# Performance work log

Measured on AMD Instinct MI355X. Metric: run time of the kernel, lower is better.

The kernel has to match this reference:

```python
import jax, jax.numpy as jnp
import numpy as np

B, N, C, H = 8, 4096, 768, 32
D = C // H  # head_dim = 24
EPS = 1e-12


def _l2norm(t):
    # F.normalize(dim=-1): t / max(||t||_2, eps)
    n = jnp.sqrt(jnp.sum(t * t, axis=-1, keepdims=True))
    return t / jnp.maximum(n, EPS)


def setup_inputs() -> dict:
    key = jax.random.key(0)
    ks = jax.random.split(key, 6)
    s_in = 1.0 / np.sqrt(C)
    return {
        "x": jax.random.normal(ks[0], (B, N, C), dtype=jnp.float32),
        "W_qkv": jax.random.uniform(ks[1], (C, 3 * C), jnp.float32, -s_in, s_in),
        "b_qkv": jax.random.uniform(ks[2], (3 * C,), jnp.float32, -s_in, s_in),
        "temperature": jnp.ones((H, 1, 1), dtype=jnp.float32),
        "W_proj": jax.random.uniform(ks[3], (C, C), jnp.float32, -s_in, s_in),
        "b_proj": jax.random.uniform(ks[4], (C,), jnp.float32, -s_in, s_in),
    }


def reference(x, W_qkv, b_qkv, temperature, W_proj, b_proj):
    b, n, c = x.shape
    qkv = x @ W_qkv + b_qkv                                  # (B,N,3C)
    qkv = qkv.reshape(b, n, 3, H, D).transpose(2, 0, 3, 1, 4)  # (3,B,H,N,D)
    q, k, v = qkv[0], qkv[1], qkv[2]                         # (B,H,N,D)
    q = jnp.swapaxes(q, -1, -2)                              # (B,H,D,N)
    k = jnp.swapaxes(k, -1, -2)
    v = jnp.swapaxes(v, -1, -2)
    q = _l2norm(q)                                           # normalize over N
    k = _l2norm(k)
    attn = jnp.einsum('bhdn,bhen->bhde', q, k) * temperature  # (B,H,D,D)
    attn = jax.nn.softmax(attn, axis=-1)
    y = jnp.einsum('bhde,bhen->bhdn', attn, v)               # (B,H,D,N)
    # Faithful to torch: (1,B,H,D,N).transpose(1,2).reshape(B,N,C)
    # == (H,B,D,N) flattened row-major into (B,N,C)
    y = jnp.transpose(y, (1, 0, 2, 3)).reshape(b, n, c)
    return y @ W_proj + b_proj
```

## Files before the change

kernel.cpp:

```cpp
#include <hip/hip_runtime.h>
#include <hip/hip_bf16.h>


#define DEVI __device__ __forceinline__

typedef __attribute__((ext_vector_type(8))) short bf16x8;
typedef __attribute__((ext_vector_type(4))) float f32x4;
typedef unsigned int u32;
typedef unsigned short u16;

DEVI u16 f2bf(float f) {
  union { float f; u32 u; } x; x.f = f;
  u32 r = x.u + 0x7FFFu + ((x.u >> 16) & 1u);
  return (u16)(r >> 16);
}

DEVI void gload_lds16(const void* g, void* l) {
  __builtin_amdgcn_global_load_lds((__attribute__((address_space(1))) void*)g,
                                   (__attribute__((address_space(3))) void*)l, 16, 0, 0);
}

__global__ __launch_bounds__(256) void cvt_kernel(const float* __restrict__ in,
                                                  u16* __restrict__ out, int n8) {
  int i = blockIdx.x * 256 + threadIdx.x;
  if (i >= n8) return;
  long o = (long)i * 8;
  float4 a = *(const float4*)(in + o);
  float4 b = *(const float4*)(in + o + 4);
  uint4 v;
  v.x = f2bf(a.x) | ((u32)f2bf(a.y) << 16);
  v.y = f2bf(a.z) | ((u32)f2bf(a.w) << 16);
  v.z = f2bf(b.x) | ((u32)f2bf(b.y) << 16);
  v.w = f2bf(b.z) | ((u32)f2bf(b.w) << 16);
  *(uint4*)(out + o) = v;
}

__global__ __launch_bounds__(256) void transpose_cvt(const float* __restrict__ W,
                                                     u16* __restrict__ Wt, int K, int N) {
  __shared__ float tile[32][33];
  int n0 = blockIdx.x * 32, k0 = blockIdx.y * 32;
  int tx = threadIdx.x, ty = threadIdx.y;
  #pragma unroll
  for (int i = 0; i < 4; ++i)
    tile[ty + 8 * i][tx] = W[(long)(k0 + ty + 8 * i) * N + n0 + tx];
  __syncthreads();
  #pragma unroll
  for (int i = 0; i < 4; ++i)
    Wt[(long)(n0 + ty + 8 * i) * K + k0 + tx] = f2bf(tile[tx][ty + 8 * i]);
}

template<int NT>
__global__ __launch_bounds__(256, 2) void gemm_w1_kernel(
    const u16* __restrict__ A, const u16* __restrict__ Bt,
    const float* __restrict__ bias, u16* __restrict__ Cout, int N) {
  constexpr int K = NT * 32;
  __shared__ __attribute__((aligned(128))) char lds[73728];

  int nbx = N >> 8;
  int nwg = gridDim.x;
  int bid = blockIdx.x;
  bid = (bid & 7) * (nwg >> 3) + (bid >> 3);
  int bx = bid % nbx, by = bid / nbx;

  int t = threadIdx.x;
  int w = t >> 6, l = t & 63;
  int wr = w >> 1, wc = w & 1;
  int l16 = l & 15, l4 = l >> 4;

  int cbb = (l4 * 16) ^ ((l16 & 8) << 2);
  int pA0 = (wr * 64 + l16) * 64 + cbb;
  int pB0 = (wc * 128 + l16) * 64 + cbb;

  int soffA[2], soffB[4];
  #pragma unroll
  for (int j = 0; j < 2; ++j) {
    int p = (j * 256 + t) * 16;
    int la = p ^ (((p >> 9) & 1) << 5);
    soffA[j] = (la >> 6) * K + ((la & 63) >> 1);
  }
  #pragma unroll
  for (int j = 0; j < 4; ++j) {
    int p = (j * 256 + t) * 16;
    int lb = p ^ (((p >> 9) & 1) << 5);
    soffB[j] = (lb >> 6) * K + ((lb & 63) >> 1);
  }

  const u16* Ag = A + (long)by * 128 * K;
  const u16* Bg = Bt + (long)bx * 256 * K;
  int sdst = w * 1024;

  f32x4 acc[4][8] = {};

#define STAGE_W1(ktile, slot)                                                  \
  { _Pragma("unroll") for (int j_ = 0; j_ < 2; ++j_)                           \
      gload_lds16(Ag + soffA[j_] + (ktile) * 32,                               \
                  lds + (slot) * 8192 + j_ * 4096 + sdst);                     \
    _Pragma("unroll") for (int j_ = 0; j_ < 4; ++j_)                           \
      gload_lds16(Bg + soffB[j_] + (ktile) * 32,                               \
                  lds + 24576 + (slot) * 16384 + j_ * 4096 + sdst); }

  STAGE_W1(0, 0);
  STAGE_W1(1, 1);

  #pragma unroll
  for (int kt = 0; kt < NT; ++kt) {
    int rs = kt % 3;
    if (kt + 2 < NT) {
      STAGE_W1(kt + 2, (kt + 2) % 3);
      asm volatile("s_waitcnt vmcnt(12)" ::: "memory");
    } else if (kt + 2 == NT) {
      asm volatile("s_waitcnt vmcnt(6)" ::: "memory");
    } else {
      asm volatile("s_waitcnt vmcnt(0)" ::: "memory");
    }
    __builtin_amdgcn_sched_barrier(0);
    __builtin_amdgcn_s_barrier();
    __builtin_amdgcn_sched_barrier(0);

    bf16x8 aF[4], bF[8];
    #pragma unroll
    for (int mi = 0; mi < 4; ++mi)
      aF[mi] = *(const bf16x8*)(lds + rs * 8192 + mi * 1024 + pA0);
    #pragma unroll
    for (int n = 0; n < 8; ++n)
      bF[n] = *(const bf16x8*)(lds + 24576 + rs * 16384 + n * 1024 + pB0);

    __builtin_amdgcn_s_setprio(1);
    #pragma unroll
    for (int mi = 0; mi < 4; ++mi)
      #pragma unroll
      for (int n = 0; n < 8; ++n)
        acc[mi][n] = __builtin_amdgcn_mfma_f32_16x16x32_bf16(aF[mi], bF[n], acc[mi][n], 0, 0, 0);
    __builtin_amdgcn_s_setprio(0);
    __builtin_amdgcn_s_barrier();
    __builtin_amdgcn_sched_barrier(0);
  }

  #pragma unroll
  for (int mi = 0; mi < 4; ++mi) {
    int row0 = by * 128 + wr * 64 + mi * 16 + l4 * 4;
    #pragma unroll
    for (int n = 0; n < 8; ++n) {
      int col = bx * 256 + wc * 128 + n * 16 + l16;
      float bv = bias[col];
      #pragma unroll
      for (int j = 0; j < 4; ++j) {
        long idx = (long)(row0 + j) * N + col;
        Cout[idx] = f2bf(acc[mi][n][j] + bv);
      }
    }
  }
#undef STAGE_W1
}

#define STAGE3(ktile, slot)                                                    \
  { _Pragma("unroll") for (int j_ = 0; j_ < 2; ++j_) {                         \
      gload_lds16(Ag + soffA[j_] + (ktile) * 32,                               \
                  lds + (slot) * 8192 + j_ * 4096 + sdst);                     \
      gload_lds16(Bg + soffB[j_] + (ktile) * 32,                               \
                  lds + 24576 + (slot) * 8192 + j_ * 4096 + sdst); } }

template<int NT>
__global__ __launch_bounds__(256, 3) void gemm3c_kernel(
    const u16* __restrict__ A, const u16* __restrict__ Bt,
    const float* __restrict__ bias, float* __restrict__ Cout,
    int M, int N) {
  constexpr int K = NT * 32;
  __shared__ __attribute__((aligned(128))) char lds[49152];

  int nbx = N >> 7;
  int nwg = gridDim.x;
  int bid = blockIdx.x;
  bid = (bid & 7) * (nwg >> 3) + (bid >> 3);
  int bx = bid % nbx, by = bid / nbx;

  int t = threadIdx.x;
  int w = t >> 6, l = t & 63;
  int wr = w >> 1, wc = w & 1;
  int l16 = l & 15, l4 = l >> 4;

  int cbb = (l4 * 16) ^ ((l16 & 8) << 2);
  int pA0 = (wr * 64 + l16) * 64 + cbb;
  int pB0 = (wc * 64 + l16) * 64 + cbb;

  int soffA[2], soffB[2];
  #pragma unroll
  for (int j = 0; j < 2; ++j) {
    int p = (j * 256 + t) * 16;
    int lb = p ^ (((p >> 9) & 1) << 5);
    soffA[j] = (lb >> 6) * K + ((lb & 63) >> 1);
    soffB[j] = soffA[j];
  }

  const u16* Ag = A + (long)by * 128 * K;
  const u16* Bg = Bt + (long)bx * 128 * K;
  int sdst = w * 1024;

  f32x4 acc[4][4] = {};

  STAGE3(0, 0);
  STAGE3(1, 1);

  #pragma unroll
  for (int kt = 0; kt < NT; ++kt) {
    int rs = kt % 3;
    if (kt + 2 < NT) {
      STAGE3(kt + 2, (kt + 2) % 3);
      asm volatile("s_waitcnt vmcnt(8)" ::: "memory");
    } else if (kt + 2 == NT) {
      asm volatile("s_waitcnt vmcnt(4)" ::: "memory");
    } else {
      asm volatile("s_waitcnt vmcnt(0)" ::: "memory");
    }
    __builtin_amdgcn_sched_barrier(0);
    __builtin_amdgcn_s_barrier();
    __builtin_amdgcn_sched_barrier(0);

    bf16x8 aF[4], bF[4];
    #pragma unroll
    for (int mi = 0; mi < 4; ++mi)
      aF[mi] = *(const bf16x8*)(lds + rs * 8192 + mi * 1024 + pA0);
    #pragma unroll
    for (int n = 0; n < 4; ++n)
      bF[n] = *(const bf16x8*)(lds + 24576 + rs * 8192 + n * 1024 + pB0);

    __builtin_amdgcn_s_setprio(1);
    #pragma unroll
    for (int mi = 0; mi < 4; ++mi)
      #pragma unroll
      for (int n = 0; n < 4; ++n)
        acc[mi][n] = __builtin_amdgcn_mfma_f32_16x16x32_bf16(aF[mi], bF[n], acc[mi][n], 0, 0, 0);
    __builtin_amdgcn_s_setprio(0);
    __builtin_amdgcn_s_barrier();
    __builtin_amdgcn_sched_barrier(0);
  }

  #pragma unroll
  for (int mi = 0; mi < 4; ++mi) {
    int row0 = by * 128 + wr * 64 + mi * 16 + l4 * 4;
    #pragma unroll
    for (int n = 0; n < 4; ++n) {
      int col = bx * 128 + wc * 64 + n * 16 + l16;
      float bv = bias[col];
      #pragma unroll
      for (int j = 0; j < 4; ++j) {
        long idx = (long)(row0 + j) * N + col;
        __builtin_nontemporal_store(acc[mi][n][j] + bv, Cout + idx);
      }
    }
  }
}

#define PFQK(nc, rq, rk)                                                       \
  { long cb = (long)(nc) * 589824;                                             \
    _Pragma("unroll") for (int i = 0; i < 3; ++i) {                            \
      rq[i] = *(const uint4*)(qbase + cb + offI[i]);                           \
      rk[i] = *(const uint4*)(kbase + cb + offI[i]); } }

#define WRQK(rq, rk)                                                           \
  { _Pragma("unroll") for (int i = 0; i < 3; ++i) {                            \
      const u32* pq = (const u32*)&rq[i];                                      \
      const u32* pk = (const u32*)&rk[i];                                      \
      _Pragma("unroll") for (int j = 0; j < 4; ++j) {                          \
        int d = sI[i] * 8 + 2 * j;                                             \
        qt[d][nI[i]] = (u16)pq[j]; qt[d + 1][nI[i]] = (u16)(pq[j] >> 16);      \
        kt[d][nI[i]] = (u16)pk[j]; kt[d + 1][nI[i]] = (u16)(pk[j] >> 16); } } }

#define GRAM8                                                                  \
  { _Pragma("unroll") for (int ks = 0; ks < 8; ++ks) {                         \
      int koff = ks * 32 + l4 * 8;                                             \
      bf16x8 qa = *(const bf16x8*)&qt[fm * 16 + l16][koff];                    \
      bf16x8 qb = *(const bf16x8*)&qt[fn * 16 + l16][koff];                    \
      bf16x8 ka = *(const bf16x8*)&kt[fm * 16 + l16][koff];                    \
      bf16x8 kb = *(const bf16x8*)&kt[fn * 16 + l16][koff];                    \
      accG = __builtin_amdgcn_mfma_f32_16x16x32_bf16(qa, kb, accG, 0, 0, 0);   \
      accQ = __builtin_amdgcn_mfma_f32_16x16x32_bf16(qa, qb, accQ, 0, 0, 0);   \
      accK = __builtin_amdgcn_mfma_f32_16x16x32_bf16(ka, kb, accK, 0, 0, 0); } }

__global__ __launch_bounds__(256) void gram_kernel(const u16* __restrict__ qkv,
                                                   float* __restrict__ gram) {
  __shared__ u16 qt[32][280];
  __shared__ u16 kt[32][280];

  int bid = blockIdx.x;
  int bh = bid >> 2, s = bid & 3;
  int b = bh >> 5, h = bh & 31;
  int t = threadIdx.x;
  int w = t >> 6, l = t & 63;
  int l16 = l & 15, l4 = l >> 4;
  int fm = w >> 1, fn = w & 1;

  for (int i = t; i < 32 * 280; i += 256) { qt[0][i] = 0; kt[0][i] = 0; }

  int nI[3], sI[3], offI[3];
  #pragma unroll
  for (int i = 0; i < 3; ++i) {
    int idx = t + 256 * i;
    nI[i] = idx / 3; sI[i] = idx % 3;
    offI[i] = nI[i] * 2304 + sI[i] * 8;
  }

  f32x4 accG = {}, accQ = {}, accK = {};
  const u16* qbase = qkv + (long)b * 4096 * 2304 + h * 24;
  const u16* kbase = qbase + 768;
  int c0 = s * 4;

  uint4 rq[3], rk[3];
  PFQK(c0, rq, rk);
  __syncthreads();

  #pragma unroll
  for (int c = 0; c < 4; ++c) {
    WRQK(rq, rk);
    __syncthreads();
    if (c + 1 < 4) PFQK(c0 + c + 1, rq, rk);
    GRAM8;
    __syncthreads();
  }

  float* gb = gram + (long)(bh * 4 + s) * 3072;
  int row = fm * 16 + l4 * 4, col = fn * 16 + l16;
  #pragma unroll
  for (int j = 0; j < 4; ++j) {
    gb[(row + j) * 32 + col] = accG[j];
    gb[1024 + (row + j) * 32 + col] = accQ[j];
    gb[2048 + (row + j) * 32 + col] = accK[j];
  }
}

__global__ __launch_bounds__(32) void softmax_kernel(const float* __restrict__ gram,
                                                     const float* __restrict__ temperature,
                                                     u16* __restrict__ attnb) {
  int bh = blockIdx.x;
  int h = bh & 31;
  int d = threadIdx.x;
  u16* ab = attnb + bh * 1024;
  if (d < 24) {
    const float* gb = gram + (long)bh * 12288;
    float nq2 = 0.f, row[24], nk2[24];
    #pragma unroll
    for (int e = 0; e < 24; ++e) { row[e] = 0.f; nk2[e] = 0.f; }
    #pragma unroll
    for (int s = 0; s < 4; ++s) {
      const float* gs = gb + s * 3072;
      nq2 += gs[1024 + d * 33];
      #pragma unroll
      for (int e = 0; e < 24; ++e) {
        row[e] += gs[d * 32 + e];
        nk2[e] += gs[2048 + e * 33];
      }
    }
    float nq = fmaxf(sqrtf(fmaxf(nq2, 0.f)), 1e-12f);
    float tmp = temperature[h];
    float mx = -1e30f;
    #pragma unroll
    for (int e = 0; e < 24; ++e) {
      float nk = fmaxf(sqrtf(fmaxf(nk2[e], 0.f)), 1e-12f);
      row[e] = row[e] / (nq * nk) * tmp;
      mx = fmaxf(mx, row[e]);
    }
    float ssum = 0.f;
    #pragma unroll
    for (int e = 0; e < 24; ++e) { row[e] = __expf(row[e] - mx); ssum += row[e]; }
    float inv = 1.f / ssum;
    #pragma unroll
    for (int e = 0; e < 24; ++e) ab[d * 32 + e] = f2bf(row[e] * inv);
    #pragma unroll
    for (int e = 24; e < 32; ++e) ab[d * 32 + e] = 0;
  } else {
    #pragma unroll
    for (int e = 0; e < 32; ++e) ab[d * 32 + e] = 0;
  }
}

__global__ __launch_bounds__(256) void pv_kernel(const u16* __restrict__ qkv,
                                                 const u16* __restrict__ attnb,
                                                 u16* __restrict__ yout) {
  __shared__ u16 vl[256][40];
  int bid = blockIdx.x;
  int bh = bid >> 4, c = bid & 15;
  int b = bh >> 5, h = bh & 31;
  int t = threadIdx.x;
  int w = t >> 6, l = t & 63;
  int l16 = l & 15, l4 = l >> 4;

  for (int i = t; i < 5120; i += 256) ((u32*)vl)[i] = 0;

  const u16* ab = attnb + bh * 1024;
  bf16x8 af0 = *(const bf16x8*)(ab + l16 * 32 + l4 * 8);
  bf16x8 af1 = *(const bf16x8*)(ab + (16 + l16) * 32 + l4 * 8);

  const u16* vbase = qkv + (long)b * 4096 * 2304 + h * 24 + 1536;
  uint4 rv[3];
  int nI[3], sI[3];
  #pragma unroll
  for (int i = 0; i < 3; ++i) {
    int idx = t + 256 * i;
    nI[i] = idx / 3; sI[i] = idx % 3;
    rv[i] = *(const uint4*)(vbase + (long)c * 589824 + nI[i] * 2304 + sI[i] * 8);
  }
  __syncthreads();
  #pragma unroll
  for (int i = 0; i < 3; ++i) *(uint4*)&vl[nI[i]][sI[i] * 8] = rv[i];
  __syncthreads();

  u16* ybase = yout + (long)(h * 8 + b) * 24 * 4096;
  int n0 = c * 256;
  f32x4 z = {};
  #pragma unroll
  for (int fnn = 0; fnn < 4; ++fnn) {
    int ncol = w * 64 + fnn * 16 + l16;
    bf16x8 bv = *(const bf16x8*)&vl[ncol][l4 * 8];
    f32x4 y0 = __builtin_amdgcn_mfma_f32_16x16x32_bf16(af0, bv, z, 0, 0, 0);
    f32x4 y1 = __builtin_amdgcn_mfma_f32_16x16x32_bf16(af1, bv, z, 0, 0, 0);
    int gn = n0 + ncol;
    #pragma unroll
    for (int j = 0; j < 4; ++j) {
      int d0 = l4 * 4 + j;
      ybase[(long)d0 * 4096 + gn] = f2bf(y0[j]);
      int d1 = 16 + d0;
      if (d1 < 24) ybase[(long)d1 * 4096 + gn] = f2bf(y1[j]);
    }
  }
}

extern "C" void kernel_launch(void* const* d_in, const int* in_sizes, int n_in,
                              void* d_out, int out_size, void* d_ws, size_t ws_size,
                              hipStream_t stream) {
  const float* x     = (const float*)d_in[0];
  const float* Wqkv  = (const float*)d_in[1];
  const float* bqkv  = (const float*)d_in[2];
  const float* temp  = (const float*)d_in[3];
  const float* Wproj = (const float*)d_in[4];
  const float* bproj = (const float*)d_in[5];
  float* out = (float*)d_out;

  char* ws = (char*)d_ws;
  u16*   xb    = (u16*)(ws);
  float* gram  = (float*)(ws);
  u16*   y     = (u16*)(ws);
  u16*   wqt   = (u16*)(ws + 50331648);
  u16*   attnb = (u16*)(ws + 50331648);
  u16*   wpt   = (u16*)(ws + 53870592);
  u16*   qkv   = (u16*)(ws + 55050240);

  cvt_kernel<<<12288, 256, 0, stream>>>(x, xb, 3145728);
  transpose_cvt<<<dim3(72, 24), dim3(32, 8), 0, stream>>>(Wqkv, wqt, 768, 2304);
  transpose_cvt<<<dim3(24, 24), dim3(32, 8), 0, stream>>>(Wproj, wpt, 768, 768);
  gemm_w1_kernel<24><<<2304, 256, 0, stream>>>(xb, wqt, bqkv, qkv, 2304);
  gram_kernel<<<1024, 256, 0, stream>>>(qkv, gram);
  softmax_kernel<<<256, 32, 0, stream>>>(gram, temp, attnb);
  pv_kernel<<<4096, 256, 0, stream>>>(qkv, attnb, y);
  gemm3c_kernel<24><<<1536, 256, 0, stream>>>(y, wpt, bproj, out, 32768, 768);
}
```

Baseline: 295.7 us.

## Use 512-thread QKV GEMM blocks and merge weight transpose launches

The QKV GEMM now runs 8 waves per block instead of 4 on the same 128x256 tile, so each wave computes 64x64 rather than 64x128. Accumulator registers are halved and the global-to-LDS staging work is spread across more threads. The two weight transpose-convert kernels are merged into one launch that picks Wqkv or Wproj from the block index. This trades fewer MFMAs per LDS fragment load, and so lower operand reuse, for more waves to hide latency, and it also saves one launch.

```diff
diff --git a/kernel.cpp b/kernel.cpp
--- a/kernel.cpp
+++ b/kernel.cpp
@@ -35,10 +35,16 @@
   *(uint4*)(out + o) = v;
 }
 
-__global__ __launch_bounds__(256) void transpose_cvt(const float* __restrict__ W,
-                                                     u16* __restrict__ Wt, int K, int N) {
+__global__ __launch_bounds__(256) void transpose_cvt2(const float* __restrict__ Wq,
+                                                      u16* __restrict__ Wqt,
+                                                      const float* __restrict__ Wp,
+                                                      u16* __restrict__ Wpt) {
   __shared__ float tile[32][33];
-  int n0 = blockIdx.x * 32, k0 = blockIdx.y * 32;
+  int bx = blockIdx.x;
+  const float* W; u16* Wt; int N, n0;
+  if (bx < 72) { W = Wq; Wt = Wqt; N = 2304; n0 = bx * 32; }
+  else         { W = Wp; Wt = Wpt; N = 768;  n0 = (bx - 72) * 32; }
+  int k0 = blockIdx.y * 32;
   int tx = threadIdx.x, ty = threadIdx.y;
   #pragma unroll
   for (int i = 0; i < 4; ++i)
@@ -46,13 +52,20 @@
   __syncthreads();
   #pragma unroll
   for (int i = 0; i < 4; ++i)
-    Wt[(long)(n0 + ty + 8 * i) * K + k0 + tx] = f2bf(tile[tx][ty + 8 * i]);
-}
+    Wt[(long)(n0 + ty + 8 * i) * 768 + k0 + tx] = f2bf(tile[tx][ty + 8 * i]);
+}
+
+#define STAGE_T(ktile, slot)                                                   \
+  { gload_lds16(Ag + soffA + (ktile) * 32, lds + (slot) * 8192 + sdst);        \
+    _Pragma("unroll") for (int j_ = 0; j_ < 2; ++j_)                           \
+      gload_lds16(Bg + soffB[j_] + (ktile) * 32,                               \
+                  lds + 24576 + (slot) * 16384 + j_ * 8192 + sdst); }
 
 template<int NT>
-__global__ __launch_bounds__(256, 2) void gemm_w1_kernel(
+__global__ __launch_bounds__(512, 4) void gemm2b_kernel(
     const u16* __restrict__ A, const u16* __restrict__ Bt,
-    const float* __restrict__ bias, u16* __restrict__ Cout, int N) {
+    const float* __restrict__ bias, u16* __restrict__ Cout,
+    int M, int N) {
   constexpr int K = NT * 32;
   __shared__ __attribute__((aligned(128))) char lds[73728];
 
@@ -64,23 +77,20 @@
 
   int t = threadIdx.x;
   int w = t >> 6, l = t & 63;
-  int wr = w >> 1, wc = w & 1;
+  int wr = w >> 2, wc = w & 3;
   int l16 = l & 15, l4 = l >> 4;
 
   int cbb = (l4 * 16) ^ ((l16 & 8) << 2);
   int pA0 = (wr * 64 + l16) * 64 + cbb;
-  int pB0 = (wc * 128 + l16) * 64 + cbb;
-
-  int soffA[2], soffB[4];
+  int pB0 = (wc * 64 + l16) * 64 + cbb;
+
+  int pa = t * 16;
+  int la = pa ^ (((pa >> 9) & 1) << 5);
+  int soffA = (la >> 6) * K + ((la & 63) >> 1);
+  int soffB[2];
   #pragma unroll
   for (int j = 0; j < 2; ++j) {
-    int p = (j * 256 + t) * 16;
-    int la = p ^ (((p >> 9) & 1) << 5);
-    soffA[j] = (la >> 6) * K + ((la & 63) >> 1);
-  }
-  #pragma unroll
-  for (int j = 0; j < 4; ++j) {
-    int p = (j * 256 + t) * 16;
+    int p = (j * 512 + t) * 16;
     int lb = p ^ (((p >> 9) & 1) << 5);
     soffB[j] = (lb >> 6) * K + ((lb & 63) >> 1);
   }
@@ -89,27 +99,19 @@
   const u16* Bg = Bt + (long)bx * 256 * K;
   int sdst = w * 1024;
 
-  f32x4 acc[4][8] = {};
-
-#define STAGE_W1(ktile, slot)                                                  \
-  { _Pragma("unroll") for (int j_ = 0; j_ < 2; ++j_)                           \
-      gload_lds16(Ag + soffA[j_] + (ktile) * 32,                               \
-                  lds + (slot) * 8192 + j_ * 4096 + sdst);                     \
-    _Pragma("unroll") for (int j_ = 0; j_ < 4; ++j_)                           \
-      gload_lds16(Bg + soffB[j_] + (ktile) * 32,                               \
-                  lds + 24576 + (slot) * 16384 + j_ * 4096 + sdst); }
-
-  STAGE_W1(0, 0);
-  STAGE_W1(1, 1);
+  f32x4 acc[4][4] = {};
+
+  STAGE_T(0, 0);
+  STAGE_T(1, 1);
 
   #pragma unroll
   for (int kt = 0; kt < NT; ++kt) {
     int rs = kt % 3;
     if (kt + 2 < NT) {
-      STAGE_W1(kt + 2, (kt + 2) % 3);
-      asm volatile("s_waitcnt vmcnt(12)" ::: "memory");
+      STAGE_T(kt + 2, (kt + 2) % 3);
+      asm volatile("s_waitcnt vmcnt(6)" ::: "memory");
     } else if (kt + 2 == NT) {
-      asm volatile("s_waitcnt vmcnt(6)" ::: "memory");
+      asm volatile("s_waitcnt vmcnt(3)" ::: "memory");
     } else {
       asm volatile("s_waitcnt vmcnt(0)" ::: "memory");
     }
@@ -117,19 +119,19 @@
     __builtin_amdgcn_s_barrier();
     __builtin_amdgcn_sched_barrier(0);
 
-    bf16x8 aF[4], bF[8];
+    bf16x8 aF[4], bF[4];
     #pragma unroll
     for (int mi = 0; mi < 4; ++mi)
       aF[mi] = *(const bf16x8*)(lds + rs * 8192 + mi * 1024 + pA0);
     #pragma unroll
-    for (int n = 0; n < 8; ++n)
+    for (int n = 0; n < 4; ++n)
       bF[n] = *(const bf16x8*)(lds + 24576 + rs * 16384 + n * 1024 + pB0);
 
     __builtin_amdgcn_s_setprio(1);
     #pragma unroll
     for (int mi = 0; mi < 4; ++mi)
       #pragma unroll
-      for (int n = 0; n < 8; ++n)
+      for (int n = 0; n < 4; ++n)
         acc[mi][n] = __builtin_amdgcn_mfma_f32_16x16x32_bf16(aF[mi], bF[n], acc[mi][n], 0, 0, 0);
     __builtin_amdgcn_s_setprio(0);
     __builtin_amdgcn_s_barrier();
@@ -140,8 +142,8 @@
   for (int mi = 0; mi < 4; ++mi) {
     int row0 = by * 128 + wr * 64 + mi * 16 + l4 * 4;
     #pragma unroll
-    for (int n = 0; n < 8; ++n) {
-      int col = bx * 256 + wc * 128 + n * 16 + l16;
+    for (int n = 0; n < 4; ++n) {
+      int col = bx * 256 + wc * 64 + n * 16 + l16;
       float bv = bias[col];
       #pragma unroll
       for (int j = 0; j < 4; ++j) {
@@ -150,7 +152,6 @@
       }
     }
   }
-#undef STAGE_W1
 }
 
 #define STAGE3(ktile, slot)                                                    \
@@ -445,9 +446,8 @@
   u16*   qkv   = (u16*)(ws + 55050240);
 
   cvt_kernel<<<12288, 256, 0, stream>>>(x, xb, 3145728);
-  transpose_cvt<<<dim3(72, 24), dim3(32, 8), 0, stream>>>(Wqkv, wqt, 768, 2304);
-  transpose_cvt<<<dim3(24, 24), dim3(32, 8), 0, stream>>>(Wproj, wpt, 768, 768);
-  gemm_w1_kernel<24><<<2304, 256, 0, stream>>>(xb, wqt, bqkv, qkv, 2304);
+  transpose_cvt2<<<dim3(96, 24), dim3(32, 8), 0, stream>>>(Wqkv, wqt, Wproj, wpt);
+  gemm2b_kernel<24><<<2304, 512, 0, stream>>>(xb, wqt, bqkv, qkv, 32768, 2304);
   gram_kernel<<<1024, 256, 0, stream>>>(qkv, gram);
   softmax_kernel<<<256, 32, 0, stream>>>(gram, temp, attnb);
   pv_kernel<<<4096, 256, 0, stream>>>(qkv, attnb, y);
```

New measurement: 295.7 us. Within noise of the previous version (-0.0%).
